# Performance work log

Measured on AMD Instinct MI355X. Metric: run time of the kernel, lower is better.

Reference implementation:

```python
import jax, jax.numpy as jnp
import numpy as np
from jax import lax

B, C_IN, C_OUT, KK, KS = 8, 32, 64, 4, 3
D, H, W = 32, 64, 64
PAD = 1

def setup_inputs() -> dict:
    key = jax.random.key(0)
    ks = jax.random.split(key, 12)
    s = 0.02
    return {
        "x": jax.random.normal(ks[0], (B, C_IN, D, H, W), jnp.float32),
        # K candidate conv kernels and biases
        "weight": jax.random.normal(ks[1], (KK, C_OUT, C_IN, KS, KS, KS), jnp.float32) * s,
        "cbias": jnp.zeros((KK, C_OUT), jnp.float32),
        "temperature": jnp.float32(34.0),
        # attention key path: BN(affine, eval-mode) -> GELU -> 1x1 conv (linear)
        "bn1_g": jnp.ones((C_IN,), jnp.float32),
        "bn1_b": jnp.zeros((C_IN,), jnp.float32),
        "w1": jax.random.normal(ks[2], (C_IN, C_IN), jnp.float32) * s,
        "b1": jnp.zeros((C_IN,), jnp.float32),
        "bn2_g": jnp.ones((C_IN,), jnp.float32),
        "bn2_b": jnp.zeros((C_IN,), jnp.float32),
        "w2": jax.random.normal(ks[3], (C_IN, C_IN), jnp.float32) * s,
        "b2": jnp.zeros((C_IN,), jnp.float32),
        "bn3_g": jnp.ones((C_IN,), jnp.float32),
        "bn3_b": jnp.zeros((C_IN,), jnp.float32),
        "w3": jax.random.normal(ks[4], (KK, C_IN), jnp.float32) * s,
        "b3": jnp.zeros((KK,), jnp.float32),
    }

def _attention(p, temperature, bn1_g, bn1_b, w1, b1, bn2_g, bn2_b, w2, b2, bn3_g, bn3_b, w3, b3):
    # p: [B, C] pooled features. 1x1x1 convs on 1x1x1 maps == linear layers.
    gelu = lambda t: jax.nn.gelu(t, approximate=False)  # torch nn.GELU default is erf
    a = gelu(p * bn1_g + bn1_b)          # BN (eval: rm=0, rv=1) + GELU
    a = a @ w1.T + b1
    a = gelu(a * bn2_g + bn2_b)
    a = a @ w2.T + b2
    a = a + p                            # ResidualLayer (plain add)
    a = a * bn3_g + bn3_b
    logits = a @ w3.T + b3               # [B, K]
    return jax.nn.softmax(logits / temperature, axis=1)

def reference(x, weight, cbias, temperature, bn1_g, bn1_b, w1, b1,
              bn2_g, bn2_b, w2, b2, bn3_g, bn3_b, w3, b3):
    # x: [B, C_in, D, H, W]
    p = x.mean(axis=(2, 3, 4))  # AdaptiveAvgPool3d(1)
    attn = _attention(p, temperature, bn1_g, bn1_b, w1, b1,
                      bn2_g, bn2_b, w2, b2, bn3_g, bn3_b, w3, b3)  # [B, K]
    # per-sample aggregated kernels / bias
    agg_w = jnp.einsum('bk,koidhw->boidhw', attn, weight)  # [B, O, I, k, k, k]
    agg_b = attn @ cbias                                    # [B, O]
    # grouped-conv trick (groups=B) == per-sample conv3d -> vmap over batch
    def conv1(xi, wi):
        return lax.conv_general_dilated(
            xi[None], wi, window_strides=(1, 1, 1),
            padding=[(PAD, PAD)] * 3,
            dimension_numbers=('NCDHW', 'OIDHW', 'NCDHW'))[0]
    out = jax.vmap(conv1)(x, agg_w)  # [B, O, D, H, W]
    return out + agg_b[:, :, None, None, None]
```

## Files before the change

kernel.cpp:

```cpp
#include <hip/hip_runtime.h>
#include <hip/hip_bf16.h>
#include <math.h>

#define B_   8
#define CIN  32
#define COUT 64
#define KK_  4
#define DD   32
#define HH   64
#define WW   64
#define HW   (HH*WW)
#define DHW  (DD*HH*WW)

typedef __attribute__((ext_vector_type(8)))  short bf16x8;
typedef __attribute__((ext_vector_type(16))) float f32x16;

__device__ __forceinline__ unsigned short f2bf(float f) {
    union { float f; unsigned int u; } v; v.f = f;
    return (unsigned short)((v.u + 0x7FFFu + ((v.u >> 16) & 1u)) >> 16);
}
__device__ __forceinline__ float bf2f(unsigned short s) {
    union { unsigned int u; float f; } v; v.u = ((unsigned int)s) << 16;
    return v.f;
}
__device__ __forceinline__ void gll16(const void* g, void* l) {
    __builtin_amdgcn_global_load_lds(
        (const __attribute__((address_space(1))) void*)g,
        (__attribute__((address_space(3))) void*)l, 16, 0, 0);
}

__global__ __launch_bounds__(256) void transpose_kernel(const float* __restrict__ x,
                                                        unsigned short* __restrict__ xt) {
    const int t = threadIdx.x;
    const int r = t >> 6, w = t & 63;
    const int h = (blockIdx.x << 2) + r;
    const int d = blockIdx.y, b = blockIdx.z;

    const float* xb = x + (size_t)b*CIN*DHW + (size_t)d*HW + (size_t)h*WW + w;
    unsigned int packed[CIN/2];
    #pragma unroll
    for (int c2 = 0; c2 < CIN/2; ++c2) {
        unsigned int lo = f2bf(xb[(size_t)(2*c2)   * DHW]);
        unsigned int hi = f2bf(xb[(size_t)(2*c2+1) * DHW]);
        packed[c2] = lo | (hi << 16);
    }
    char* row = (char*)xt + (size_t)((b*DD + d)*HH + h) * 4096;
    #pragma unroll
    for (int q = 0; q < 4; ++q) {
        uint4 v = make_uint4(packed[4*q], packed[4*q+1], packed[4*q+2], packed[4*q+3]);
        *(uint4*)(row + q*1024 + (((w << 4)) ^ (q << 4))) = v;
    }
}

__global__ __launch_bounds__(256) void pool2_kernel(const unsigned short* __restrict__ xt,
                                                    float* __restrict__ pblk) {
    const int t = threadIdx.x;
    const int oct = t >> 6, wi = t & 63;
    const int d = blockIdx.x, b = blockIdx.y;
    const char* base = (const char*)xt + (size_t)((b*DD + d)*HH) * 4096 + oct*1024 + wi*16;
    float acc[8];
    #pragma unroll
    for (int j = 0; j < 8; ++j) acc[j] = 0.f;
    for (int h = 0; h < HH; ++h) {
        bf16x8 v = *(const bf16x8*)(base + (size_t)h * 4096);
        #pragma unroll
        for (int j = 0; j < 8; ++j) acc[j] += bf2f((unsigned short)v[j]);
    }
    #pragma unroll
    for (int off = 32; off > 0; off >>= 1) {
        #pragma unroll
        for (int j = 0; j < 8; ++j) acc[j] += __shfl_xor(acc[j], off);
    }
    if ((t & 63) == 0) {
        #pragma unroll
        for (int j = 0; j < 8; ++j)
            pblk[(b*DD + d)*CIN + oct*8 + j] = acc[j];
    }
}

__device__ __forceinline__ float gelu_erf(float v) {
    return 0.5f * v * (1.f + erff(v * 0.70710678118654752f));
}

__global__ void attn_kernel(const float* __restrict__ pblk,
                            const float* __restrict__ temperature,
                            const float* __restrict__ bn1_g, const float* __restrict__ bn1_b,
                            const float* __restrict__ w1,    const float* __restrict__ b1,
                            const float* __restrict__ bn2_g, const float* __restrict__ bn2_b,
                            const float* __restrict__ w2,    const float* __restrict__ b2,
                            const float* __restrict__ bn3_g, const float* __restrict__ bn3_b,
                            const float* __restrict__ w3,    const float* __restrict__ b3,
                            const float* __restrict__ cbias,
                            float* __restrict__ attn_out, float* __restrict__ aggb_out) {
    __shared__ float A[B_][CIN], A2[B_][CIN];
    __shared__ float L[B_][KK_], ATT[B_][KK_];
    const int t = threadIdx.x;
    const int b = t >> 5, c = t & 31;

    float pv = 0.f;
    for (int dd = 0; dd < DD; ++dd) pv += pblk[(b*DD + dd)*CIN + c];
    pv *= (1.f / (float)DHW);

    A[b][c] = gelu_erf(pv * bn1_g[c] + bn1_b[c]);
    __syncthreads();

    float s = b1[c];
    for (int j = 0; j < CIN; ++j) s += A[b][j] * w1[c*CIN + j];
    A2[b][c] = gelu_erf(s * bn2_g[c] + bn2_b[c]);
    __syncthreads();

    float s2 = b2[c];
    for (int j = 0; j < CIN; ++j) s2 += A2[b][j] * w2[c*CIN + j];
    s2 += pv;
    s2 = s2 * bn3_g[c] + bn3_b[c];
    __syncthreads();
    A[b][c] = s2;
    __syncthreads();

    if (c < KK_) {
        float lv = b3[c];
        for (int j = 0; j < CIN; ++j) lv += A[b][j] * w3[c*CIN + j];
        L[b][c] = lv;
    }
    __syncthreads();

    const float T = temperature[0];
    if (c < KK_) {
        float m = fmaxf(fmaxf(L[b][0], L[b][1]), fmaxf(L[b][2], L[b][3]));
        float e = expf((L[b][c] - m) / T);
        float den = 0.f;
        for (int j = 0; j < KK_; ++j) den += expf((L[b][j] - m) / T);
        float av = e / den;
        ATT[b][c] = av;
        attn_out[b*KK_ + c] = av;
    }
    __syncthreads();

    for (int o = c; o < COUT; o += CIN) {
        float sb = 0.f;
        for (int k = 0; k < KK_; ++k) sb += ATT[b][k] * cbias[k*COUT + o];
        aggb_out[b*COUT + o] = sb;
    }
}

__global__ void aggw_kernel(const float* __restrict__ weight,
                            const float* __restrict__ attn,
                            unsigned short* __restrict__ wt) {
    const int idx = blockIdx.x * 256 + threadIdx.x;
    const int ci   = idx & 31;
    const int co   = (idx >> 5) & 63;
    int r          = idx >> 11;
    const int kpos = r % 27;
    const int b    = r / 27;
    float s = 0.f;
    #pragma unroll
    for (int k = 0; k < KK_; ++k)
        s += attn[b*KK_ + k] * weight[((k*COUT + co)*CIN + ci)*27 + kpos];
    wt[idx] = f2bf(s);
}

__global__ __launch_bounds__(512, 4) void conv_mfma(const unsigned short* __restrict__ xt,
                                                    const unsigned short* __restrict__ wt,
                                                    const float* __restrict__ aggb,
                                                    float* __restrict__ out) {
    __shared__ char smem[18 * 4096];
    const int t    = threadIdx.x;
    const int lane = t & 63;
    const int wid  = t >> 6;
    const int cv   = wid & 1;
    const int wv   = (wid >> 1) & 1;
    const int dv   = wid >> 2;
    const int lw   = lane & 31, lh = lane >> 5;

    const int id = blockIdx.x;
    const int b  = id & 7;
    const int h  = (id >> 3) & 63;
    const int d0 = ((id >> 9) & 7) << 2;

    const char* xb  = (const char*)xt + (size_t)(b*DD)*HH*4096;
    const char* wtb = (const char*)wt + (size_t)b * 27 * 4096;

    auto stage_row = [&](int zo, int ho) {
        const int zd = d0 - 1 + zo, yh = h - 1 + ho;
        char* dst = smem + (size_t)((zo*3 + ho) << 12);
        if ((unsigned)zd < DD && (unsigned)yh < HH) {
            const char* src = xb + (size_t)(zd*HH + yh)*4096 + lane*16;
            #pragma unroll
            for (int q = 0; q < 4; ++q) gll16(src + (q << 10), dst + (q << 10));
        } else {
            #pragma unroll
            for (int q = 0; q < 4; ++q)
                *(uint4*)(dst + (q << 10) + lane*16) = make_uint4(0u,0u,0u,0u);
        }
    };

    for (int rid = wid; rid < 18; rid += 8)
        stage_row(rid / 3, rid % 3);
    __syncthreads();

    f32x16 acc[2];
    acc[0] = (f32x16){};
    acc[1] = (f32x16){};

    const int a_off = (cv << 11) + lw*64 + lh*16;
    const int o0 = lh, o1 = 2 + lh;
    const bf16x8 bz = {};

    #pragma unroll
    for (int kh = 0; kh < 3; ++kh) {
        #pragma unroll
        for (int kw = 0; kw < 3; ++kw) {
            bf16x8 av[3][2];
            #pragma unroll
            for (int kd = 0; kd < 3; ++kd) {
                const char* wk = wtb + (size_t)(((kd*3 + kh)*3 + kw) << 12);
                av[kd][0] = *(const bf16x8*)(wk + a_off);
                av[kd][1] = *(const bf16x8*)(wk + 32 + a_off);
            }

            const int wp  = (wv << 5) + lw + kw - 1;
            const bool oob = ((unsigned)wp >= (unsigned)WW);
            const int wpc = oob ? ((wp < 0) ? 0 : (WW - 1)) : wp;
            const int sw0 = (o0 << 10) + ((wpc << 4) ^ (o0 << 4));
            const int sw1 = (o1 << 10) + ((wpc << 4) ^ (o1 << 4));

            bf16x8 bc[4][2];
            #pragma unroll
            for (int j = 0; j < 4; ++j) {
                const int rb = ((((dv << 1) + j)*3 + kh) << 12);
                bf16x8 v0 = *(const bf16x8*)&smem[rb + sw0];
                bf16x8 v1 = *(const bf16x8*)&smem[rb + sw1];
                bc[j][0] = oob ? bz : v0;
                bc[j][1] = oob ? bz : v1;
            }
            #pragma unroll
            for (int kd = 0; kd < 3; ++kd) {
                #pragma unroll
                for (int r = 0; r < 2; ++r) {
                    const int j = r + kd;
                    acc[r] = __builtin_amdgcn_mfma_f32_32x32x16_bf16(av[kd][0], bc[j][0], acc[r], 0, 0, 0);
                    acc[r] = __builtin_amdgcn_mfma_f32_32x32x16_bf16(av[kd][1], bc[j][1], acc[r], 0, 0, 0);
                }
            }
        }
    }

    const float* ab = aggb + b*COUT;
    const int sp0 = h*WW + (wv << 5) + lw;
    #pragma unroll
    for (int reg = 0; reg < 16; ++reg) {
        const int co = (cv << 5) + (reg & 3) + ((reg >> 2) << 3) + (lh << 2);
        const float bb = ab[co];
        float* oc = out + ((size_t)(b*COUT + co))*DHW + sp0;
        #pragma unroll
        for (int r = 0; r < 2; ++r)
            oc[(size_t)(d0 + (dv << 1) + r)*HW] = acc[r][reg] + bb;
    }
}

extern "C" void kernel_launch(void* const* d_in, const int* in_sizes, int n_in,
                              void* d_out, int out_size, void* d_ws, size_t ws_size,
                              hipStream_t stream) {
    const float* x           = (const float*)d_in[0];
    const float* weight      = (const float*)d_in[1];
    const float* cbias       = (const float*)d_in[2];
    const float* temperature = (const float*)d_in[3];
    const float* bn1_g       = (const float*)d_in[4];
    const float* bn1_b       = (const float*)d_in[5];
    const float* w1          = (const float*)d_in[6];
    const float* b1          = (const float*)d_in[7];
    const float* bn2_g       = (const float*)d_in[8];
    const float* bn2_b       = (const float*)d_in[9];
    const float* w2          = (const float*)d_in[10];
    const float* b2          = (const float*)d_in[11];
    const float* bn3_g       = (const float*)d_in[12];
    const float* bn3_b       = (const float*)d_in[13];
    const float* w3          = (const float*)d_in[14];
    const float* b3          = (const float*)d_in[15];
    float* out = (float*)d_out;

    char* ws = (char*)d_ws;
    float*          attn = (float*)(ws + 1024);
    float*          aggb = (float*)(ws + 2048);
    float*          pblk = (float*)(ws + 16384);
    unsigned short* wt   = (unsigned short*)(ws + 65536);
    unsigned short* xt   = (unsigned short*)(ws + (1u << 20));

    transpose_kernel<<<dim3(HH/4, DD, B_), 256, 0, stream>>>(x, xt);
    pool2_kernel<<<dim3(DD, B_), 256, 0, stream>>>(xt, pblk);
    attn_kernel<<<1, 256, 0, stream>>>(pblk, temperature,
                                       bn1_g, bn1_b, w1, b1,
                                       bn2_g, bn2_b, w2, b2,
                                       bn3_g, bn3_b, w3, b3,
                                       cbias, attn, aggb);
    aggw_kernel<<<(B_*27*COUT*CIN)/256, 256, 0, stream>>>(weight, attn, wt);
    conv_mfma<<<dim3(64*8*8), 512, 0, stream>>>(xt, wt, aggb, out);
}
```

Measured before the change: 202.5 us.

## Fuse pooling into transpose and restructure conv MFMA loop with zero-row LDS

```diff
diff --git a/kernel.cpp b/kernel.cpp
--- a/kernel.cpp
+++ b/kernel.cpp
@@ -19,10 +19,6 @@
     union { float f; unsigned int u; } v; v.f = f;
     return (unsigned short)((v.u + 0x7FFFu + ((v.u >> 16) & 1u)) >> 16);
 }
-__device__ __forceinline__ float bf2f(unsigned short s) {
-    union { unsigned int u; float f; } v; v.u = ((unsigned int)s) << 16;
-    return v.f;
-}
 __device__ __forceinline__ void gll16(const void* g, void* l) {
     __builtin_amdgcn_global_load_lds(
         (const __attribute__((address_space(1))) void*)g,
@@ -30,18 +26,24 @@
 }
 
 __global__ __launch_bounds__(256) void transpose_kernel(const float* __restrict__ x,
-                                                        unsigned short* __restrict__ xt) {
+                                                        unsigned short* __restrict__ xt,
+                                                        float* __restrict__ pblk) {
     const int t = threadIdx.x;
     const int r = t >> 6, w = t & 63;
-    const int h = (blockIdx.x << 2) + r;
+    const int hb = blockIdx.x;
+    const int h = (hb << 2) + r;
     const int d = blockIdx.y, b = blockIdx.z;
 
     const float* xb = x + (size_t)b*CIN*DHW + (size_t)d*HW + (size_t)h*WW + w;
+    float f[CIN];
+    #pragma unroll
+    for (int c = 0; c < CIN; ++c) f[c] = xb[(size_t)c * DHW];
+
     unsigned int packed[CIN/2];
     #pragma unroll
     for (int c2 = 0; c2 < CIN/2; ++c2) {
-        unsigned int lo = f2bf(xb[(size_t)(2*c2)   * DHW]);
-        unsigned int hi = f2bf(xb[(size_t)(2*c2+1) * DHW]);
+        unsigned int lo = f2bf(f[2*c2]);
+        unsigned int hi = f2bf(f[2*c2+1]);
         packed[c2] = lo | (hi << 16);
     }
     char* row = (char*)xt + (size_t)((b*DD + d)*HH + h) * 4096;
@@ -50,32 +52,18 @@
         uint4 v = make_uint4(packed[4*q], packed[4*q+1], packed[4*q+2], packed[4*q+3]);
         *(uint4*)(row + q*1024 + (((w << 4)) ^ (q << 4))) = v;
     }
-}
-
-__global__ __launch_bounds__(256) void pool2_kernel(const unsigned short* __restrict__ xt,
-                                                    float* __restrict__ pblk) {
-    const int t = threadIdx.x;
-    const int oct = t >> 6, wi = t & 63;
-    const int d = blockIdx.x, b = blockIdx.y;
-    const char* base = (const char*)xt + (size_t)((b*DD + d)*HH) * 4096 + oct*1024 + wi*16;
-    float acc[8];
-    #pragma unroll
-    for (int j = 0; j < 8; ++j) acc[j] = 0.f;
-    for (int h = 0; h < HH; ++h) {
-        bf16x8 v = *(const bf16x8*)(base + (size_t)h * 4096);
-        #pragma unroll
-        for (int j = 0; j < 8; ++j) acc[j] += bf2f((unsigned short)v[j]);
-    }
+
     #pragma unroll
     for (int off = 32; off > 0; off >>= 1) {
         #pragma unroll
-        for (int j = 0; j < 8; ++j) acc[j] += __shfl_xor(acc[j], off);
-    }
-    if ((t & 63) == 0) {
-        #pragma unroll
-        for (int j = 0; j < 8; ++j)
-            pblk[(b*DD + d)*CIN + oct*8 + j] = acc[j];
-    }
+        for (int c = 0; c < CIN; ++c) f[c] += __shfl_xor(f[c], off);
+    }
+    __shared__ float ws4[4][CIN];
+    if ((t & 63) < CIN) ws4[r][t & 63] = f[t & 63];
+    __syncthreads();
+    if (t < CIN)
+        pblk[(size_t)((b*DD + d)*16 + hb)*CIN + t] =
+            ws4[0][t] + ws4[1][t] + ws4[2][t] + ws4[3][t];
 }
 
 __device__ __forceinline__ float gelu_erf(float v) {
@@ -98,7 +86,7 @@
     const int b = t >> 5, c = t & 31;
 
     float pv = 0.f;
-    for (int dd = 0; dd < DD; ++dd) pv += pblk[(b*DD + dd)*CIN + c];
+    for (int i = 0; i < DD*16; ++i) pv += pblk[(size_t)(b*DD*16 + i)*CIN + c];
     pv *= (1.f / (float)DHW);
 
     A[b][c] = gelu_erf(pv * bn1_g[c] + bn1_b[c]);
@@ -163,7 +151,7 @@
                                                     const unsigned short* __restrict__ wt,
                                                     const float* __restrict__ aggb,
                                                     float* __restrict__ out) {
-    __shared__ char smem[18 * 4096];
+    __shared__ char smem[19 * 4096];
     const int t    = threadIdx.x;
     const int lane = t & 63;
     const int wid  = t >> 6;
@@ -179,6 +167,8 @@
 
     const char* xb  = (const char*)xt + (size_t)(b*DD)*HH*4096;
     const char* wtb = (const char*)wt + (size_t)b * 27 * 4096;
+
+    if (t < 256) *(uint4*)&smem[18*4096 + t*16] = make_uint4(0u,0u,0u,0u);
 
     auto stage_row = [&](int zo, int ho) {
         const int zd = d0 - 1 + zo, yh = h - 1 + ho;
@@ -193,7 +183,6 @@
                 *(uint4*)(dst + (q << 10) + lane*16) = make_uint4(0u,0u,0u,0u);
         }
     };
-
     for (int rid = wid; rid < 18; rid += 8)
         stage_row(rid / 3, rid % 3);
     __syncthreads();
@@ -204,44 +193,71 @@
 
     const int a_off = (cv << 11) + lw*64 + lh*16;
     const int o0 = lh, o1 = 2 + lh;
-    const bf16x8 bz = {};
+    const int z0 = 18*4096 + (o0 << 10) + (lw << 4);
+    const int z1 = 18*4096 + (o1 << 10) + (lw << 4);
 
     #pragma unroll
     for (int kh = 0; kh < 3; ++kh) {
+        bf16x8 av[2][3][2];
+        #pragma unroll
+        for (int kw2 = 0; kw2 < 2; ++kw2)
+            #pragma unroll
+            for (int kd = 0; kd < 3; ++kd) {
+                const char* wk = wtb + (size_t)(((kd*3 + kh)*3 + kw2) << 12);
+                av[kw2][kd][0] = *(const bf16x8*)(wk + a_off);
+                av[kw2][kd][1] = *(const bf16x8*)(wk + 32 + a_off);
+            }
+        asm volatile("" ::: "memory");
+
         #pragma unroll
         for (int kw = 0; kw < 3; ++kw) {
-            bf16x8 av[3][2];
-            #pragma unroll
-            for (int kd = 0; kd < 3; ++kd) {
-                const char* wk = wtb + (size_t)(((kd*3 + kh)*3 + kw) << 12);
-                av[kd][0] = *(const bf16x8*)(wk + a_off);
-                av[kd][1] = *(const bf16x8*)(wk + 32 + a_off);
+            if (kw == 2) {
+                #pragma unroll
+                for (int kd = 0; kd < 3; ++kd) {
+                    const char* wk = wtb + (size_t)(((kd*3 + kh)*3 + 2) << 12);
+                    av[0][kd][0] = *(const bf16x8*)(wk + a_off);
+                    av[0][kd][1] = *(const bf16x8*)(wk + 32 + a_off);
+                }
+                asm volatile("" ::: "memory");
             }
+            const int ai = (kw == 2) ? 0 : kw;
 
             const int wp  = (wv << 5) + lw + kw - 1;
             const bool oob = ((unsigned)wp >= (unsigned)WW);
-            const int wpc = oob ? ((wp < 0) ? 0 : (WW - 1)) : wp;
+            const int wpc = oob ? 0 : wp;
             const int sw0 = (o0 << 10) + ((wpc << 4) ^ (o0 << 4));
             const int sw1 = (o1 << 10) + ((wpc << 4) ^ (o1 << 4));
 
-            bf16x8 bc[4][2];
-            #pragma unroll
-            for (int j = 0; j < 4; ++j) {
-                const int rb = ((((dv << 1) + j)*3 + kh) << 12);
-                bf16x8 v0 = *(const bf16x8*)&smem[rb + sw0];
-                bf16x8 v1 = *(const bf16x8*)&smem[rb + sw1];
-                bc[j][0] = oob ? bz : v0;
-                bc[j][1] = oob ? bz : v1;
-            }
-            #pragma unroll
-            for (int kd = 0; kd < 3; ++kd) {
-                #pragma unroll
-                for (int r = 0; r < 2; ++r) {
-                    const int j = r + kd;
-                    acc[r] = __builtin_amdgcn_mfma_f32_32x32x16_bf16(av[kd][0], bc[j][0], acc[r], 0, 0, 0);
-                    acc[r] = __builtin_amdgcn_mfma_f32_32x32x16_bf16(av[kd][1], bc[j][1], acc[r], 0, 0, 0);
-                }
-            }
+            const int rb0 = (((dv << 1) + 0)*3 + kh) << 12;
+            const int rb1 = (((dv << 1) + 1)*3 + kh) << 12;
+            const int rb2 = (((dv << 1) + 2)*3 + kh) << 12;
+            const int rb3 = (((dv << 1) + 3)*3 + kh) << 12;
+
+            bf16x8 bA0 = *(const bf16x8*)&smem[oob ? z0 : rb0 + sw0];
+            bf16x8 bA1 = *(const bf16x8*)&smem[oob ? z1 : rb0 + sw1];
+            bf16x8 bB0 = *(const bf16x8*)&smem[oob ? z0 : rb1 + sw0];
+            bf16x8 bB1 = *(const bf16x8*)&smem[oob ? z1 : rb1 + sw1];
+
+            acc[0] = __builtin_amdgcn_mfma_f32_32x32x16_bf16(av[ai][0][0], bA0, acc[0], 0, 0, 0);
+            acc[0] = __builtin_amdgcn_mfma_f32_32x32x16_bf16(av[ai][0][1], bA1, acc[0], 0, 0, 0);
+            acc[1] = __builtin_amdgcn_mfma_f32_32x32x16_bf16(av[ai][0][0], bB0, acc[1], 0, 0, 0);
+            acc[1] = __builtin_amdgcn_mfma_f32_32x32x16_bf16(av[ai][0][1], bB1, acc[1], 0, 0, 0);
+
+            bf16x8 bC0 = *(const bf16x8*)&smem[oob ? z0 : rb2 + sw0];
+            bf16x8 bC1 = *(const bf16x8*)&smem[oob ? z1 : rb2 + sw1];
+
+            acc[0] = __builtin_amdgcn_mfma_f32_32x32x16_bf16(av[ai][1][0], bB0, acc[0], 0, 0, 0);
+            acc[0] = __builtin_amdgcn_mfma_f32_32x32x16_bf16(av[ai][1][1], bB1, acc[0], 0, 0, 0);
+            acc[1] = __builtin_amdgcn_mfma_f32_32x32x16_bf16(av[ai][1][0], bC0, acc[1], 0, 0, 0);
+            acc[1] = __builtin_amdgcn_mfma_f32_32x32x16_bf16(av[ai][1][1], bC1, acc[1], 0, 0, 0);
+
+            bf16x8 bD0 = *(const bf16x8*)&smem[oob ? z0 : rb3 + sw0];
+            bf16x8 bD1 = *(const bf16x8*)&smem[oob ? z1 : rb3 + sw1];
+
+            acc[0] = __builtin_amdgcn_mfma_f32_32x32x16_bf16(av[ai][2][0], bC0, acc[0], 0, 0, 0);
+            acc[0] = __builtin_amdgcn_mfma_f32_32x32x16_bf16(av[ai][2][1], bC1, acc[0], 0, 0, 0);
+            acc[1] = __builtin_amdgcn_mfma_f32_32x32x16_bf16(av[ai][2][0], bD0, acc[1], 0, 0, 0);
+            acc[1] = __builtin_amdgcn_mfma_f32_32x32x16_bf16(av[ai][2][1], bD1, acc[1], 0, 0, 0);
         }
     }
 
@@ -281,13 +297,12 @@
 
     char* ws = (char*)d_ws;
     float*          attn = (float*)(ws + 1024);
-    float*          aggb = (float*)(ws + 2048);
-    float*          pblk = (float*)(ws + 16384);
-    unsigned short* wt   = (unsigned short*)(ws + 65536);
-    unsigned short* xt   = (unsigned short*)(ws + (1u << 20));
-
-    transpose_kernel<<<dim3(HH/4, DD, B_), 256, 0, stream>>>(x, xt);
-    pool2_kernel<<<dim3(DD, B_), 256, 0, stream>>>(xt, pblk);
+    float*          aggb = (float*)(ws + 4096);
+    float*          pblk = (float*)(ws + 65536);
+    unsigned short* wt   = (unsigned short*)(ws + 622592);
+    unsigned short* xt   = (unsigned short*)(ws + 1507328);
+
+    transpose_kernel<<<dim3(HH/4, DD, B_), 256, 0, stream>>>(x, xt, pblk);
     attn_kernel<<<1, 256, 0, stream>>>(pblk, temperature,
                                        bn1_g, bn1_b, w1, b1,
                                        bn2_g, bn2_b, w2, b2,
```

Result: no change. 203.6 us (+0.6%).
